# Kernel optimization log

Hardware: AMD Instinct MI355X
Metric: run time of the kernel (lower is better)

Reference implementation:

```python
import jax, jax.numpy as jnp
import numpy as np

N_POINTS = 2_000_000
IN_CH = 10
OUT_CH = 32  # out_channels // 2 since last_layer=False
NUM_PILLARS = 30_000
BN_EPS = 1e-3


def setup_inputs() -> dict:
    key = jax.random.key(0)
    k1, k2, k3, k4, k5 = jax.random.split(key, 5)
    inputs = jax.random.normal(k1, (N_POINTS, IN_CH), dtype=jnp.float32)
    unq_inv = jnp.sort(jax.random.randint(k2, (N_POINTS,), 0, NUM_PILLARS, dtype=jnp.int64))
    W = jax.random.normal(k3, (OUT_CH, IN_CH), dtype=jnp.float32) * 0.1
    gamma = jax.random.uniform(k4, (OUT_CH,), dtype=jnp.float32, minval=0.5, maxval=1.5)
    beta = jax.random.normal(k5, (OUT_CH,), dtype=jnp.float32) * 0.1
    running_mean = jnp.zeros((OUT_CH,), dtype=jnp.float32)
    running_var = jnp.ones((OUT_CH,), dtype=jnp.float32)
    return {
        "inputs": inputs,
        "unq_inv": unq_inv,
        "num_out_inds": NUM_PILLARS,
        "W": W,
        "gamma": gamma,
        "beta": beta,
        "running_mean": running_mean,
        "running_var": running_var,
    }


def reference(inputs, unq_inv, num_out_inds, W, gamma, beta, running_mean, running_var):
    # linear (no bias): [N, in] x [out, in]^T -> [N, out]
    x = jnp.einsum("ni,oi->no", inputs, W)
    # BatchNorm1d (eval / running stats), eps=1e-3
    inv_std = jax.lax.rsqrt(running_var + BN_EPS)
    x = (x - running_mean) * (inv_std * gamma) + beta
    x = jax.nn.relu(x)
    # scatter_max into a zero-initialized buffer: since x >= 0 post-ReLU,
    # this equals max(segment_max, 0); empty segments stay 0.
    x_max = jax.ops.segment_max(x, unq_inv, num_segments=num_out_inds)
    x_max = jnp.maximum(x_max, 0.0)
    # gather back per point and concat -> [N, 2*out]
    return jnp.concatenate([x, x_max[unq_inv, :]], axis=1)
```

## Files before the change

kernel.cpp:

```cpp
#include <hip/hip_runtime.h>

#define IN_CH       10
#define OUT_CH      32
#define NUM_PILLARS 30000
#define BN_EPS      1e-3f

#define BLOCK 256
#define PPB   7
#define CHUNK 512

typedef float fv4 __attribute__((ext_vector_type(4)));
typedef float fv2 __attribute__((ext_vector_type(2)));

__global__ void k_start(const int* __restrict__ inv, int* __restrict__ ps, int n) {
    const int p = blockIdx.x * blockDim.x + threadIdx.x;
    if (p >= n) return;
    const int b = inv[p];
    const int a = (p == 0) ? -1 : inv[p - 1];
    for (int pid = a + 1; pid <= b; ++pid) ps[pid] = p;
    if (p == n - 1)
        for (int pid = b + 1; pid <= NUM_PILLARS; ++pid) ps[pid] = n;
}

__global__ __launch_bounds__(BLOCK) void k_pillar(
    const float* __restrict__ in,
    const int*   __restrict__ inv,
    const float* __restrict__ W,
    const float* __restrict__ gamma,
    const float* __restrict__ beta,
    const float* __restrict__ mean,
    const float* __restrict__ var,
    const int*   __restrict__ ps,
    float*       __restrict__ out,
    int n)
{
    __shared__ float s_sc[OUT_CH], s_b[OUT_CH];
    __shared__ float s_Wf[OUT_CH * IN_CH];
    __shared__ float s_in[CHUNK * 16];
    __shared__ int   s_pid[CHUNK];
    __shared__ unsigned s_pm[PPB * OUT_CH];

    const int t = threadIdx.x;
    const int P0 = blockIdx.x * PPB;
    const int P1 = min(P0 + PPB, NUM_PILLARS);

    if (t < OUT_CH) {
        float sc = rsqrtf(var[t] + BN_EPS) * gamma[t];
        s_sc[t] = sc;
        s_b[t]  = beta[t] - mean[t] * sc;
    }
    if (t < PPB * OUT_CH) s_pm[t] = 0u;
    __syncthreads();
    for (int i = t; i < OUT_CH * IN_CH; i += BLOCK)
        s_Wf[i] = W[i] * s_sc[i / IN_CH];
    __syncthreads();

    const int start = ps[P0];
    const int end   = ps[P1];

    const int strip = t >> 3;
    const int c0 = (t & 7) * 4;
    const int sb = strip & 3;

    float w0[IN_CH], w1[IN_CH], w2[IN_CH], w3[IN_CH];
    #pragma unroll
    for (int i = 0; i < IN_CH; ++i) {
        w0[i] = s_Wf[(c0 + 0) * IN_CH + i];
        w1[i] = s_Wf[(c0 + 1) * IN_CH + i];
        w2[i] = s_Wf[(c0 + 2) * IN_CH + i];
        w3[i] = s_Wf[(c0 + 3) * IN_CH + i];
    }
    const float b0 = s_b[c0], b1 = s_b[c0 + 1], b2 = s_b[c0 + 2], b3 = s_b[c0 + 3];

    for (int cbase = start; cbase < end; cbase += CHUNK) {
        const int cnt = min(CHUNK, end - cbase);
        __syncthreads();
        #pragma unroll
        for (int k = 0; k < (CHUNK * IN_CH) / (BLOCK * 2); ++k) {
            const int f = (t + k * BLOCK) * 2;
            fv2 v = {0.f, 0.f};
            if (f < cnt * IN_CH)
                v = *reinterpret_cast<const fv2*>(in + (long)cbase * IN_CH + f);
            const int r = f / IN_CH, c = f - r * IN_CH;
            const int sw = ((c >> 2) ^ ((r >> 4) & 3)) << 2;
            s_in[r * 16 + sw + (c & 3)]     = v.x;
            s_in[r * 16 + sw + (c & 3) + 1] = v.y;
        }
        #pragma unroll
        for (int k = 0; k < CHUNK / BLOCK; ++k) {
            const int pl = t + k * BLOCK;
            s_pid[pl] = (pl < cnt) ? inv[cbase + pl] : -1;
        }
        __syncthreads();

        int curPid = -1;
        float m0 = 0.f, m1 = 0.f, m2 = 0.f, m3 = 0.f;
        #pragma unroll
        for (int s = 0; s < 16; ++s) {
            const int pl = strip * 16 + s;
            if (pl < cnt) {
                const int pid = s_pid[pl];
                const fv4 x0 = *reinterpret_cast<const fv4*>(&s_in[pl * 16 + ((0 ^ sb) << 2)]);
                const fv4 x1 = *reinterpret_cast<const fv4*>(&s_in[pl * 16 + ((1 ^ sb) << 2)]);
                const fv2 x2 = *reinterpret_cast<const fv2*>(&s_in[pl * 16 + ((2 ^ sb) << 2)]);
                const float xi[IN_CH] = {x0[0], x0[1], x0[2], x0[3],
                                         x1[0], x1[1], x1[2], x1[3], x2[0], x2[1]};
                float a0 = b0, a1 = b1, a2 = b2, a3 = b3;
                #pragma unroll
                for (int i = 0; i < IN_CH; ++i) {
                    a0 = fmaf(xi[i], w0[i], a0);
                    a1 = fmaf(xi[i], w1[i], a1);
                    a2 = fmaf(xi[i], w2[i], a2);
                    a3 = fmaf(xi[i], w3[i], a3);
                }
                a0 = fmaxf(a0, 0.f); a1 = fmaxf(a1, 0.f);
                a2 = fmaxf(a2, 0.f); a3 = fmaxf(a3, 0.f);

                fv4 v = {a0, a1, a2, a3};
                __builtin_nontemporal_store(v,
                    reinterpret_cast<fv4*>(out + (size_t)(cbase + pl) * 64 + c0));

                if (pid != curPid) {
                    if (curPid >= 0) {
                        unsigned* q = &s_pm[(curPid - P0) * OUT_CH + c0];
                        atomicMax(q + 0, __float_as_uint(m0));
                        atomicMax(q + 1, __float_as_uint(m1));
                        atomicMax(q + 2, __float_as_uint(m2));
                        atomicMax(q + 3, __float_as_uint(m3));
                    }
                    curPid = pid;
                    m0 = a0; m1 = a1; m2 = a2; m3 = a3;
                } else {
                    m0 = fmaxf(m0, a0); m1 = fmaxf(m1, a1);
                    m2 = fmaxf(m2, a2); m3 = fmaxf(m3, a3);
                }
            }
        }
        if (curPid >= 0) {
            unsigned* q = &s_pm[(curPid - P0) * OUT_CH + c0];
            atomicMax(q + 0, __float_as_uint(m0));
            atomicMax(q + 1, __float_as_uint(m1));
            atomicMax(q + 2, __float_as_uint(m2));
            atomicMax(q + 3, __float_as_uint(m3));
        }
    }
    __syncthreads();

    const int slot8 = t & 7;
    const int pofs  = t >> 3;
    for (int cbase = start; cbase < end; cbase += CHUNK) {
        const int cnt = min(CHUNK, end - cbase);
        for (int it = 0; it < CHUNK / 32; ++it) {
            const int pl = it * 32 + pofs;
            if (pl < cnt) {
                const int lp = inv[cbase + pl] - P0;
                fv4 v = *reinterpret_cast<const fv4*>(&s_pm[lp * OUT_CH + slot8 * 4]);
                __builtin_nontemporal_store(v,
                    reinterpret_cast<fv4*>(out + (size_t)(cbase + pl) * 64 + 32 + slot8 * 4));
            }
        }
    }
}

extern "C" void kernel_launch(void* const* d_in, const int* in_sizes, int n_in,
                              void* d_out, int out_size, void* d_ws, size_t ws_size,
                              hipStream_t stream) {
    const float* in    = (const float*)d_in[0];
    const int*   inv   = (const int*)d_in[1];
    const float* W     = (const float*)d_in[3];
    const float* gamma = (const float*)d_in[4];
    const float* beta  = (const float*)d_in[5];
    const float* mean  = (const float*)d_in[6];
    const float* var   = (const float*)d_in[7];
    float* out = (float*)d_out;
    int*   ps  = (int*)d_ws;

    const int n = in_sizes[1];

    k_start<<<(n + BLOCK - 1) / BLOCK, BLOCK, 0, stream>>>(inv, ps, n);

    const int nblk = (NUM_PILLARS + PPB - 1) / PPB;
    k_pillar<<<nblk, BLOCK, 0, stream>>>(in, inv, W, gamma, beta, mean, var,
                                         ps, out, n);
}
```

Baseline: 111.6 us.

## Replace pillar-start kernel with in-block binary search and reuse staged pillar ids

Drops the separate k_start launch that built a pillar-start table. Each block now binary-searches the sorted index array for its first and last pillar. The gather phase reuses the pillar ids already staged in shared memory when the block's range fits in one chunk. Input loads are also marked nontemporal. This removes a kernel launch and a 2M-thread pass, at the cost of about 21 dependent global reads per block for the search.

```diff
diff --git a/kernel.cpp b/kernel.cpp
--- a/kernel.cpp
+++ b/kernel.cpp
@@ -12,16 +12,6 @@
 typedef float fv4 __attribute__((ext_vector_type(4)));
 typedef float fv2 __attribute__((ext_vector_type(2)));
 
-__global__ void k_start(const int* __restrict__ inv, int* __restrict__ ps, int n) {
-    const int p = blockIdx.x * blockDim.x + threadIdx.x;
-    if (p >= n) return;
-    const int b = inv[p];
-    const int a = (p == 0) ? -1 : inv[p - 1];
-    for (int pid = a + 1; pid <= b; ++pid) ps[pid] = p;
-    if (p == n - 1)
-        for (int pid = b + 1; pid <= NUM_PILLARS; ++pid) ps[pid] = n;
-}
-
 __global__ __launch_bounds__(BLOCK) void k_pillar(
     const float* __restrict__ in,
     const int*   __restrict__ inv,
@@ -30,7 +20,6 @@
     const float* __restrict__ beta,
     const float* __restrict__ mean,
     const float* __restrict__ var,
-    const int*   __restrict__ ps,
     float*       __restrict__ out,
     int n)
 {
@@ -39,10 +28,22 @@
     __shared__ float s_in[CHUNK * 16];
     __shared__ int   s_pid[CHUNK];
     __shared__ unsigned s_pm[PPB * OUT_CH];
+    __shared__ int   s_se[2];
 
     const int t = threadIdx.x;
     const int P0 = blockIdx.x * PPB;
     const int P1 = min(P0 + PPB, NUM_PILLARS);
+
+    {
+        const int key = (t & 1) ? P1 : P0;
+        int lo = 0, hi = n;
+        while (lo < hi) {
+            const int mid = (lo + hi) >> 1;
+            const int v = inv[mid];
+            if (v < key) lo = mid + 1; else hi = mid;
+        }
+        if (t < 2) s_se[t] = lo;
+    }
 
     if (t < OUT_CH) {
         float sc = rsqrtf(var[t] + BN_EPS) * gamma[t];
@@ -55,8 +56,8 @@
         s_Wf[i] = W[i] * s_sc[i / IN_CH];
     __syncthreads();
 
-    const int start = ps[P0];
-    const int end   = ps[P1];
+    const int start = s_se[0];
+    const int end   = s_se[1];
 
     const int strip = t >> 3;
     const int c0 = (t & 7) * 4;
@@ -80,7 +81,8 @@
             const int f = (t + k * BLOCK) * 2;
             fv2 v = {0.f, 0.f};
             if (f < cnt * IN_CH)
-                v = *reinterpret_cast<const fv2*>(in + (long)cbase * IN_CH + f);
+                v = __builtin_nontemporal_load(
+                        reinterpret_cast<const fv2*>(in + (long)cbase * IN_CH + f));
             const int r = f / IN_CH, c = f - r * IN_CH;
             const int sw = ((c >> 2) ^ ((r >> 4) & 3)) << 2;
             s_in[r * 16 + sw + (c & 3)]     = v.x;
@@ -146,6 +148,7 @@
     }
     __syncthreads();
 
+    const bool one_chunk = (end - start) <= CHUNK;
     const int slot8 = t & 7;
     const int pofs  = t >> 3;
     for (int cbase = start; cbase < end; cbase += CHUNK) {
@@ -153,7 +156,8 @@
         for (int it = 0; it < CHUNK / 32; ++it) {
             const int pl = it * 32 + pofs;
             if (pl < cnt) {
-                const int lp = inv[cbase + pl] - P0;
+                const int pid = one_chunk ? s_pid[pl] : inv[cbase + pl];
+                const int lp = pid - P0;
                 fv4 v = *reinterpret_cast<const fv4*>(&s_pm[lp * OUT_CH + slot8 * 4]);
                 __builtin_nontemporal_store(v,
                     reinterpret_cast<fv4*>(out + (size_t)(cbase + pl) * 64 + 32 + slot8 * 4));
@@ -173,13 +177,10 @@
     const float* mean  = (const float*)d_in[6];
     const float* var   = (const float*)d_in[7];
     float* out = (float*)d_out;
-    int*   ps  = (int*)d_ws;
 
     const int n = in_sizes[1];
 
-    k_start<<<(n + BLOCK - 1) / BLOCK, BLOCK, 0, stream>>>(inv, ps, n);
-
     const int nblk = (NUM_PILLARS + PPB - 1) / PPB;
     k_pillar<<<nblk, BLOCK, 0, stream>>>(in, inv, W, gamma, beta, mean, var,
-                                         ps, out, n);
+                                         out, n);
 }
```

Measured after the change: 191.3 us. 1.71x slower.
